# Optimization experiments

Hardware: AMD Instinct MI355X
Metric: run time of the kernel (lower is better)

The kernel has to match this reference:

```python
import jax, jax.numpy as jnp
import numpy as np

CONF = 0.3      # confidence threshold (NMS.conf)
IOU = 0.6       # IoU threshold (NMS.iou)
MAX_WH = 4096.0 # class-offset trick for per-class NMS
K = 2048        # max candidates entering NMS (yolov5-style cap)
MAX_DET = 300   # max detections kept per image (fixed output size)


def setup_inputs() -> dict:
    key = jax.random.key(0)
    kxy, kwh, kobj, kcls = jax.random.split(key, 4)
    B, N, NC = 8, 25200, 80
    # realistic raw predictions: xywh in pixel units for a 640x640 image
    xy = jax.random.uniform(kxy, (B, N, 2), minval=0.0, maxval=640.0)
    wh = jax.random.uniform(kwh, (B, N, 2), minval=2.0, maxval=160.0)
    obj = jax.random.uniform(kobj, (B, N, 1))
    cls = jax.random.uniform(kcls, (B, N, NC))
    x = jnp.concatenate([xy, wh, obj, cls], axis=-1)  # [B, N, 5+NC]
    return {"x": x}


def _xywh2xyxy(b):
    xy, half = b[..., :2], b[..., 2:4] * 0.5
    return jnp.concatenate([xy - half, xy + half], axis=-1)


def _pairwise_iou(boxes):  # boxes: [K, 4] xyxy -> [K, K]
    lt = jnp.maximum(boxes[:, None, :2], boxes[None, :, :2])
    rb = jnp.minimum(boxes[:, None, 2:], boxes[None, :, 2:])
    inter = jnp.clip(rb - lt, 0.0).prod(-1)
    area = (boxes[:, 2] - boxes[:, 0]) * (boxes[:, 3] - boxes[:, 1])
    return inter / (area[:, None] + area[None, :] - inter + 1e-9)


def _nms_single(pred):  # pred: [N, 5+NC]
    obj = pred[:, 4]
    cls_conf = pred[:, 5:] * obj[:, None]          # conf = obj * cls prob
    conf = cls_conf.max(-1)
    cls_id = jnp.argmax(cls_conf, -1)
    valid = (obj > CONF) & (conf > CONF)           # candidate + final threshold
    boxes = _xywh2xyxy(pred[:, :4])
    scores = jnp.where(valid, conf, -1.0)
    top_s, idx = jax.lax.top_k(scores, K)          # cap candidates, sorted desc
    boxes_k = boxes[idx]
    cls_k = cls_id[idx]
    valid_k = top_s > 0.0
    # offset boxes by class so NMS is per-class
    shifted = boxes_k + cls_k[:, None].astype(boxes_k.dtype) * MAX_WH
    iou = _pairwise_iou(shifted)                   # [K, K]
    order = jnp.arange(K)

    def body(keep, i):  # greedy suppression in score order
        active = keep[i] & valid_k[i]
        sup = (iou[i] > IOU) & (order > i)
        keep = jnp.where(active, keep & ~sup, keep)
        return keep, None

    keep, _ = jax.lax.scan(body, jnp.ones((K,), bool), order)
    keep = keep & valid_k
    final_s = jnp.where(keep, top_s, -1.0)
    det_s, det_i = jax.lax.top_k(final_s, MAX_DET)
    dets = jnp.concatenate(
        [boxes_k[det_i], top_s[det_i][:, None],
         cls_k[det_i][:, None].astype(boxes_k.dtype)], axis=-1)  # [MAX_DET, 6]
    return dets, det_s > 0.0


def reference(x):
    # returns (dets [B, MAX_DET, 6] = xyxy,conf,cls ; valid mask [B, MAX_DET])
    return jax.vmap(_nms_single)(x)
```

## Files before the change

### kernel.cpp

```cpp
#include <hip/hip_runtime.h>
#include <hip/hip_bf16.h>

#define B 8
#define N 25200
#define ROW 85
#define NC 80
#define K 2048
#define MAXDET 300
#define NBUCKET 16384
#define CAND_CAP 4096
#define NCHUNK 32
#define STILE 64

__global__ void __launch_bounds__(256)
nms_score_kernel(const float* __restrict__ x,
                 float* __restrict__ scores,
                 int* __restrict__ cls_id) {
    int b = blockIdx.y;
    int i0 = blockIdx.x * STILE;
    int rows = N - i0; if (rows > STILE) rows = STILE;
    __shared__ float lx[STILE * ROW];
    {
        const float4* s4 = (const float4*)(x + ((size_t)b * N + i0) * ROW);
        float4* d4 = (float4*)lx;
        int nv = rows * ROW / 4;
        for (int k = threadIdx.x; k < nv; k += 256) d4[k] = s4[k];
    }
    __syncthreads();
    int g = threadIdx.x >> 2;
    int q = threadIdx.x & 3;
    if (g >= rows) return;
    const float* p = lx + g * ROW;
    float obj = p[4];
    float best = -1e30f;
    int bc = 127;
    if (obj > 0.3f) {
        #pragma unroll
        for (int k = 0; k < 20; ++k) {
            int c = q + 4 * k;
            float v = __fmul_rn(p[5 + c], obj);
            if (v > best) { best = v; bc = c; }
        }
    }
    #pragma unroll
    for (int m = 1; m < 4; m <<= 1) {
        float ov = __shfl_xor(best, m, 64);
        int   oc = __shfl_xor(bc, m, 64);
        if (ov > best || (ov == best && oc < bc)) { best = ov; bc = oc; }
    }
    if (q == 0) {
        int i = i0 + g;
        float score = (obj > 0.3f && best > 0.3f) ? best : -1.0f;
        scores[b * N + i] = score;
        cls_id[b * N + i] = (bc == 127) ? 0 : bc;
    }
}

__global__ void __launch_bounds__(1024, 1)
nms_select_kernel(const float* __restrict__ scores,
                  const float* __restrict__ x,
                  const int* __restrict__ cls_id,
                  float* __restrict__ top_s,
                  float* __restrict__ boxes,
                  int* __restrict__ clsk,
                  float* __restrict__ shifted,
                  float* __restrict__ area,
                  unsigned long long* __restrict__ keepbits) {
    __shared__ unsigned loff[NBUCKET];
    __shared__ unsigned lcnt16[NBUCKET / 2];
    __shared__ unsigned long long lk[CAND_CAP];
    __shared__ unsigned wsum[16];

    int b = blockIdx.x;
    int t = threadIdx.x;
    int ln = t & 63, wv = t >> 6;
    constexpr int NITER = (N + 1023) / 1024;

    if (t < NCHUNK) keepbits[b * NCHUNK + t] = 0ULL;

    {
        uint4 z = {0u, 0u, 0u, 0u};
        uint4* d1 = (uint4*)loff;
        for (int k = t; k < NBUCKET / 4; k += 1024) d1[k] = z;
        uint4* d2 = (uint4*)lcnt16;
        for (int k = t; k < NBUCKET / 8; k += 1024) d2[k] = z;
    }
    for (int k = t; k < CAND_CAP; k += 1024) lk[k] = 0ULL;
    __syncthreads();

    float sreg[NITER];
    #pragma unroll
    for (int r = 0; r < NITER; ++r) {
        int i = t + r * 1024;
        float s = (i < N) ? scores[b * N + i] : -1.0f;
        sreg[r] = s;
        if (s > 0.0f) {
            int q = (int)(__fmul_rn(s, 16384.0f));
            if (q > NBUCKET - 1) q = NBUCKET - 1;
            atomicAdd(&loff[q], 1u);
        }
    }
    __syncthreads();

    unsigned v[16];
    int base_j = t * 16;
    unsigned A4 = (unsigned)(NBUCKET - 16 - base_j) / 4;
    {
        uint4 u0 = ((uint4*)loff)[A4 + 0];
        uint4 u1 = ((uint4*)loff)[A4 + 1];
        uint4 u2 = ((uint4*)loff)[A4 + 2];
        uint4 u3 = ((uint4*)loff)[A4 + 3];
        unsigned u[16] = {u0.x,u0.y,u0.z,u0.w, u1.x,u1.y,u1.z,u1.w,
                          u2.x,u2.y,u2.z,u2.w, u3.x,u3.y,u3.z,u3.w};
        #pragma unroll
        for (int k = 0; k < 16; ++k) v[k] = u[15 - k];
    }
    unsigned S = 0;
    #pragma unroll
    for (int k = 0; k < 16; ++k) S += v[k];
    unsigned pref = S;
    #pragma unroll
    for (int o = 1; o < 64; o <<= 1) { unsigned u = __shfl_up(pref, o, 64); if (ln >= o) pref += u; }
    if (ln == 63) wsum[wv] = pref;
    __syncthreads();
    unsigned wbase = 0;
    for (int w = 0; w < wv; ++w) wbase += wsum[w];
    unsigned running = wbase + pref - S;
    {
        unsigned o[16];
        #pragma unroll
        for (int k = 0; k < 16; ++k) { o[15 - k] = running; running += v[k]; }
        ((uint4*)loff)[A4 + 0] = make_uint4(o[0],  o[1],  o[2],  o[3]);
        ((uint4*)loff)[A4 + 1] = make_uint4(o[4],  o[5],  o[6],  o[7]);
        ((uint4*)loff)[A4 + 2] = make_uint4(o[8],  o[9],  o[10], o[11]);
        ((uint4*)loff)[A4 + 3] = make_uint4(o[12], o[13], o[14], o[15]);
    }
    __syncthreads();

    #pragma unroll
    for (int r = 0; r < NITER; ++r) {
        float s = sreg[r];
        if (s > 0.0f) {
            int i = t + r * 1024;
            int q = (int)(__fmul_rn(s, 16384.0f));
            if (q > NBUCKET - 1) q = NBUCKET - 1;
            unsigned start = loff[q];
            if (start < CAND_CAP) {
                unsigned sh = (q & 1) * 16;
                unsigned old = atomicAdd(&lcnt16[q >> 1], 1u << sh);
                unsigned rank = (old >> sh) & 0xFFFFu;
                unsigned pos = start + rank;
                if (pos < CAND_CAP) {
                    unsigned long long key =
                        ((unsigned long long)__float_as_uint(s) << 32) | (unsigned)(~i);
                    lk[pos] = key;
                }
            }
        }
    }
    __syncthreads();

    for (int q = t; q < NBUCKET; q += 1024) {
        unsigned start = loff[q];
        if (start < CAND_CAP) {
            unsigned c = (lcnt16[q >> 1] >> ((q & 1) * 16)) & 0xFFFFu;
            unsigned m = c;
            if (m > CAND_CAP - start) m = CAND_CAP - start;
            if (m >= 2) {
                for (unsigned a = start + 1; a < start + m; ++a) {
                    unsigned long long kv = lk[a];
                    unsigned p2 = a;
                    while (p2 > start && lk[p2 - 1] < kv) { lk[p2] = lk[p2 - 1]; --p2; }
                    lk[p2] = kv;
                }
            }
        }
    }
    __syncthreads();

    for (int r = t; r < K; r += 1024) {
        unsigned long long key = lk[r];
        float s;
        int idx;
        float x1, y1, x2, y2;
        int c;
        if (key == 0ULL) {
            s = -1.0f; x1 = y1 = x2 = y2 = 0.0f; c = 0;
        } else {
            s = __uint_as_float((unsigned)(key >> 32));
            idx = (int)(~(unsigned)key);
            const float* p = x + ((size_t)b * N + idx) * ROW;
            float cx = p[0], cy = p[1], w = p[2], h = p[3];
            float hx = __fmul_rn(w, 0.5f);
            float hy = __fmul_rn(h, 0.5f);
            x1 = __fsub_rn(cx, hx); y1 = __fsub_rn(cy, hy);
            x2 = __fadd_rn(cx, hx); y2 = __fadd_rn(cy, hy);
            c = cls_id[b * N + idx];
        }
        int o = b * K + r;
        top_s[o] = s;
        boxes[o * 4 + 0] = x1; boxes[o * 4 + 1] = y1;
        boxes[o * 4 + 2] = x2; boxes[o * 4 + 3] = y2;
        clsk[o] = c;
        float sh = __fmul_rn((float)c, 4096.0f);
        float sx1 = __fadd_rn(x1, sh), sy1 = __fadd_rn(y1, sh);
        float sx2 = __fadd_rn(x2, sh), sy2 = __fadd_rn(y2, sh);
        shifted[o * 4 + 0] = sx1; shifted[o * 4 + 1] = sy1;
        shifted[o * 4 + 2] = sx2; shifted[o * 4 + 3] = sy2;
        area[o] = __fmul_rn(__fsub_rn(sx2, sx1), __fsub_rn(sy2, sy1));
    }
}

__global__ void __launch_bounds__(64)
nms_class_kernel(const float* __restrict__ top_s,
                 const int* __restrict__ clsk,
                 const float* __restrict__ shifted,
                 const float* __restrict__ area,
                 unsigned long long* __restrict__ keepbits) {
    int c = blockIdx.x, b = blockIdx.y;
    int t = threadIdx.x;
    unsigned long long below = (t == 0) ? 0ULL : (~0ULL >> (64 - t));

    __shared__ int srank[K];
    __shared__ unsigned long long skeep[NCHUNK];

    int n = 0;
    for (int ch = 0; ch < NCHUNK; ++ch) {
        int r = ch * 64 + t;
        bool sel = (clsk[b * K + r] == c) && (top_s[b * K + r] > 0.0f);
        unsigned long long m = __ballot(sel);
        if (sel) srank[n + __popcll(m & below)] = r;
        n += __popcll(m);
    }
    __syncthreads();
    if (n == 0) return;

    if (n <= 64) {
        float x1 = 0.f, y1 = 0.f, x2 = 0.f, y2 = 0.f, ar = 0.f;
        int r = -1;
        if (t < n) {
            r = srank[t];
            const float* sb = shifted + ((size_t)b * K + r) * 4;
            x1 = sb[0]; y1 = sb[1]; x2 = sb[2]; y2 = sb[3];
            ar = area[b * K + r];
        }
        unsigned long long keepw = (n == 64) ? ~0ULL : ((1ULL << n) - 1ULL);
        for (int i = 0; i < n; ++i) {
            if (!((keepw >> i) & 1ULL)) continue;
            float bx1 = __shfl(x1, i, 64), by1 = __shfl(y1, i, 64);
            float bx2 = __shfl(x2, i, 64), by2 = __shfl(y2, i, 64);
            float ba  = __shfl(ar, i, 64);
            bool cond = false;
            if (t > i && t < n) {
                float lx = fmaxf(bx1, x1), ly = fmaxf(by1, y1);
                float rx = fminf(bx2, x2), ry = fminf(by2, y2);
                float w = fmaxf(__fsub_rn(rx, lx), 0.0f);
                float h = fmaxf(__fsub_rn(ry, ly), 0.0f);
                float inter = __fmul_rn(w, h);
                float denom = __fadd_rn(__fsub_rn(__fadd_rn(ba, ar), inter), 1e-9f);
                cond = __fdiv_rn(inter, denom) > 0.6f;
            }
            keepw &= ~__ballot(cond);
        }
        if (t < n && ((keepw >> t) & 1ULL))
            atomicOr(&keepbits[b * NCHUNK + (r >> 6)], 1ULL << (r & 63));
        return;
    }

    for (int w = t; w < NCHUNK; w += 64) {
        int lo = w * 64;
        unsigned long long vw;
        if (n >= lo + 64)      vw = ~0ULL;
        else if (n <= lo)      vw = 0ULL;
        else                   vw = (1ULL << (n - lo)) - 1ULL;
        skeep[w] = vw;
    }
    __syncthreads();
    for (int i = 0; i < n; ++i) {
        if (!((skeep[i >> 6] >> (i & 63)) & 1ULL)) continue;
        int ri = srank[i];
        const float* sbi = shifted + ((size_t)b * K + ri) * 4;
        float bx1 = sbi[0], by1 = sbi[1], bx2 = sbi[2], by2 = sbi[3];
        float ba = area[b * K + ri];
        int jb_hi = (n - 1) >> 6;
        for (int jb2 = (i + 1) >> 6; jb2 <= jb_hi; ++jb2) {
            int j = jb2 * 64 + t;
            bool cond = false;
            if (j > i && j < n) {
                int rj = srank[j];
                const float* sbj = shifted + ((size_t)b * K + rj) * 4;
                float x1 = sbj[0], y1 = sbj[1], x2 = sbj[2], y2 = sbj[3];
                float arj = area[b * K + rj];
                float lx = fmaxf(bx1, x1), ly = fmaxf(by1, y1);
                float rx = fminf(bx2, x2), ry = fminf(by2, y2);
                float w = fmaxf(__fsub_rn(rx, lx), 0.0f);
                float h = fmaxf(__fsub_rn(ry, ly), 0.0f);
                float inter = __fmul_rn(w, h);
                float denom = __fadd_rn(__fsub_rn(__fadd_rn(ba, arj), inter), 1e-9f);
                cond = __fdiv_rn(inter, denom) > 0.6f;
            }
            unsigned long long sup = __ballot(cond);
            if (t == 0) skeep[jb2] &= ~sup;
        }
        __syncthreads();
    }
    for (int j = t; j < n; j += 64) {
        if ((skeep[j >> 6] >> (j & 63)) & 1ULL) {
            int r = srank[j];
            atomicOr(&keepbits[b * NCHUNK + (r >> 6)], 1ULL << (r & 63));
        }
    }
}

__global__ void __launch_bounds__(64)
nms_out_kernel(const unsigned long long* __restrict__ keepbits,
               const float* __restrict__ top_s,
               const float* __restrict__ boxes,
               const int* __restrict__ clsk,
               float* __restrict__ out) {
    int b = blockIdx.x;
    int lane = threadIdx.x;
    __shared__ unsigned long long kept[NCHUNK];
    if (lane < NCHUNK) kept[lane] = keepbits[b * NCHUNK + lane];
    __syncthreads();

    int total = 0;
    for (int c = 0; c < NCHUNK; ++c) total += __popcll(kept[c]);

    float* dets  = out + (size_t)b * MAXDET * 6;
    float* flags = out + (size_t)B * MAXDET * 6 + (size_t)b * MAXDET;
    unsigned long long below = (lane == 0) ? 0ULL : (~0ULL >> (64 - lane));
    int kc = 0, nc2 = 0;
    for (int c = 0; c < NCHUNK; ++c) {
        int i = c * 64 + lane;
        unsigned long long m = kept[c];
        bool k = ((m >> lane) & 1ULL) != 0ULL;
        int pc = __popcll(m);
        int slot = k ? (kc + __popcll(m & below))
                     : (total + nc2 + __popcll((~m) & below));
        if (slot < MAXDET) {
            int o = b * K + i;
            dets[slot * 6 + 0] = boxes[o * 4 + 0];
            dets[slot * 6 + 1] = boxes[o * 4 + 1];
            dets[slot * 6 + 2] = boxes[o * 4 + 2];
            dets[slot * 6 + 3] = boxes[o * 4 + 3];
            dets[slot * 6 + 4] = top_s[o];
            dets[slot * 6 + 5] = (float)clsk[o];
            flags[slot] = k ? 1.0f : 0.0f;
        }
        kc += pc;
        nc2 += 64 - pc;
    }
}

extern "C" void kernel_launch(void* const* d_in, const int* in_sizes, int n_in,
                              void* d_out, int out_size, void* d_ws, size_t ws_size,
                              hipStream_t stream) {
    const float* x = (const float*)d_in[0];
    float* out = (float*)d_out;

    char* ws = (char*)d_ws;
    size_t off = 0;
    auto alloc = [&](size_t bytes) -> void* {
        void* p = ws + off;
        off += bytes;
        off = (off + 255) & ~(size_t)255;
        return p;
    };

    float*    scores = (float*)    alloc((size_t)B * N * 4);
    int*      cls_id = (int*)      alloc((size_t)B * N * 4);
    float*    top_s  = (float*)    alloc((size_t)B * K * 4);
    float*    boxes  = (float*)    alloc((size_t)B * K * 4 * 4);
    int*      clsk   = (int*)      alloc((size_t)B * K * 4);
    float*    shifted= (float*)    alloc((size_t)B * K * 4 * 4);
    float*    area   = (float*)    alloc((size_t)B * K * 4);
    unsigned long long* keepbits = (unsigned long long*) alloc((size_t)B * NCHUNK * 8);
    (void)ws_size;

    nms_score_kernel<<<dim3((N + STILE - 1) / STILE, B), 256, 0, stream>>>(x, scores, cls_id);
    nms_select_kernel<<<B, 1024, 0, stream>>>(scores, x, cls_id,
                                              top_s, boxes, clsk, shifted, area, keepbits);
    nms_class_kernel<<<dim3(NC, B), 64, 0, stream>>>(top_s, clsk, shifted, area, keepbits);
    nms_out_kernel<<<B, 64, 0, stream>>>(keepbits, top_s, boxes, clsk, out);
}
```

Baseline: 145.4 us.

## Fuse select, per-class NMS and output into one LDS-resident kernel

Merges the candidate selection, per-class greedy NMS and output compaction kernels into a single 1024-thread block per image. Intermediate boxes, scores and keep bits stay in shared memory through unions, removing three launches and their global round trips. Each of the 16 waves now handles five classes instead of one block per class, so per-class parallelism drops from 640 blocks to 8 blocks of 16 waves. Classes with more than 64 candidates scan all K entries serially, which could be slow if such classes occur.

```diff
diff --git a/kernel.cpp b/kernel.cpp
--- a/kernel.cpp
+++ b/kernel.cpp
@@ -57,35 +57,45 @@
 }
 
 __global__ void __launch_bounds__(1024, 1)
-nms_select_kernel(const float* __restrict__ scores,
-                  const float* __restrict__ x,
-                  const int* __restrict__ cls_id,
-                  float* __restrict__ top_s,
-                  float* __restrict__ boxes,
-                  int* __restrict__ clsk,
-                  float* __restrict__ shifted,
-                  float* __restrict__ area,
-                  unsigned long long* __restrict__ keepbits) {
-    __shared__ unsigned loff[NBUCKET];
-    __shared__ unsigned lcnt16[NBUCKET / 2];
-    __shared__ unsigned long long lk[CAND_CAP];
+nms_fused_kernel(const float* __restrict__ scores,
+                 const float* __restrict__ x,
+                 const int* __restrict__ cls_id,
+                 float* __restrict__ out) {
+    __shared__ __align__(16) union {
+        struct { unsigned loff[NBUCKET]; unsigned lcnt16[NBUCKET / 2]; } s1;
+        struct {
+            float sx1[K], sy1[K], sx2[K], sy2[K];
+            float bx1[K], by1[K], bx2[K], by2[K];
+            float sar[K];
+            float ssc[K];
+            int   scl[K];
+        } s2;
+    } U;
+    __shared__ __align__(16) union {
+        unsigned long long lk[CAND_CAP];
+        struct {
+            int tmp64[16][64];
+            unsigned long long wmemb[16][NCHUNK];
+            unsigned long long wkeep[16][NCHUNK];
+            unsigned kept32[2 * NCHUNK];
+        } s3;
+    } V;
     __shared__ unsigned wsum[16];
 
     int b = blockIdx.x;
     int t = threadIdx.x;
     int ln = t & 63, wv = t >> 6;
+    unsigned long long below = (ln == 0) ? 0ULL : (~0ULL >> (64 - ln));
     constexpr int NITER = (N + 1023) / 1024;
-
-    if (t < NCHUNK) keepbits[b * NCHUNK + t] = 0ULL;
 
     {
         uint4 z = {0u, 0u, 0u, 0u};
-        uint4* d1 = (uint4*)loff;
+        uint4* d1 = (uint4*)U.s1.loff;
         for (int k = t; k < NBUCKET / 4; k += 1024) d1[k] = z;
-        uint4* d2 = (uint4*)lcnt16;
+        uint4* d2 = (uint4*)U.s1.lcnt16;
         for (int k = t; k < NBUCKET / 8; k += 1024) d2[k] = z;
     }
-    for (int k = t; k < CAND_CAP; k += 1024) lk[k] = 0ULL;
+    for (int k = t; k < CAND_CAP; k += 1024) V.lk[k] = 0ULL;
     __syncthreads();
 
     float sreg[NITER];
@@ -97,7 +107,7 @@
         if (s > 0.0f) {
             int q = (int)(__fmul_rn(s, 16384.0f));
             if (q > NBUCKET - 1) q = NBUCKET - 1;
-            atomicAdd(&loff[q], 1u);
+            atomicAdd(&U.s1.loff[q], 1u);
         }
     }
     __syncthreads();
@@ -106,10 +116,10 @@
     int base_j = t * 16;
     unsigned A4 = (unsigned)(NBUCKET - 16 - base_j) / 4;
     {
-        uint4 u0 = ((uint4*)loff)[A4 + 0];
-        uint4 u1 = ((uint4*)loff)[A4 + 1];
-        uint4 u2 = ((uint4*)loff)[A4 + 2];
-        uint4 u3 = ((uint4*)loff)[A4 + 3];
+        uint4 u0 = ((uint4*)U.s1.loff)[A4 + 0];
+        uint4 u1 = ((uint4*)U.s1.loff)[A4 + 1];
+        uint4 u2 = ((uint4*)U.s1.loff)[A4 + 2];
+        uint4 u3 = ((uint4*)U.s1.loff)[A4 + 3];
         unsigned u[16] = {u0.x,u0.y,u0.z,u0.w, u1.x,u1.y,u1.z,u1.w,
                           u2.x,u2.y,u2.z,u2.w, u3.x,u3.y,u3.z,u3.w};
         #pragma unroll
@@ -130,10 +140,10 @@
         unsigned o[16];
         #pragma unroll
         for (int k = 0; k < 16; ++k) { o[15 - k] = running; running += v[k]; }
-        ((uint4*)loff)[A4 + 0] = make_uint4(o[0],  o[1],  o[2],  o[3]);
-        ((uint4*)loff)[A4 + 1] = make_uint4(o[4],  o[5],  o[6],  o[7]);
-        ((uint4*)loff)[A4 + 2] = make_uint4(o[8],  o[9],  o[10], o[11]);
-        ((uint4*)loff)[A4 + 3] = make_uint4(o[12], o[13], o[14], o[15]);
+        ((uint4*)U.s1.loff)[A4 + 0] = make_uint4(o[0],  o[1],  o[2],  o[3]);
+        ((uint4*)U.s1.loff)[A4 + 1] = make_uint4(o[4],  o[5],  o[6],  o[7]);
+        ((uint4*)U.s1.loff)[A4 + 2] = make_uint4(o[8],  o[9],  o[10], o[11]);
+        ((uint4*)U.s1.loff)[A4 + 3] = make_uint4(o[12], o[13], o[14], o[15]);
     }
     __syncthreads();
 
@@ -144,16 +154,16 @@
             int i = t + r * 1024;
             int q = (int)(__fmul_rn(s, 16384.0f));
             if (q > NBUCKET - 1) q = NBUCKET - 1;
-            unsigned start = loff[q];
+            unsigned start = U.s1.loff[q];
             if (start < CAND_CAP) {
                 unsigned sh = (q & 1) * 16;
-                unsigned old = atomicAdd(&lcnt16[q >> 1], 1u << sh);
+                unsigned old = atomicAdd(&U.s1.lcnt16[q >> 1], 1u << sh);
                 unsigned rank = (old >> sh) & 0xFFFFu;
                 unsigned pos = start + rank;
                 if (pos < CAND_CAP) {
                     unsigned long long key =
                         ((unsigned long long)__float_as_uint(s) << 32) | (unsigned)(~i);
-                    lk[pos] = key;
+                    V.lk[pos] = key;
                 }
             }
         }
@@ -161,17 +171,17 @@
     __syncthreads();
 
     for (int q = t; q < NBUCKET; q += 1024) {
-        unsigned start = loff[q];
+        unsigned start = U.s1.loff[q];
         if (start < CAND_CAP) {
-            unsigned c = (lcnt16[q >> 1] >> ((q & 1) * 16)) & 0xFFFFu;
+            unsigned c = (U.s1.lcnt16[q >> 1] >> ((q & 1) * 16)) & 0xFFFFu;
             unsigned m = c;
             if (m > CAND_CAP - start) m = CAND_CAP - start;
             if (m >= 2) {
                 for (unsigned a = start + 1; a < start + m; ++a) {
-                    unsigned long long kv = lk[a];
+                    unsigned long long kv = V.lk[a];
                     unsigned p2 = a;
-                    while (p2 > start && lk[p2 - 1] < kv) { lk[p2] = lk[p2 - 1]; --p2; }
-                    lk[p2] = kv;
+                    while (p2 > start && V.lk[p2 - 1] < kv) { V.lk[p2] = V.lk[p2 - 1]; --p2; }
+                    V.lk[p2] = kv;
                 }
             }
         }
@@ -179,7 +189,7 @@
     __syncthreads();
 
     for (int r = t; r < K; r += 1024) {
-        unsigned long long key = lk[r];
+        unsigned long long key = V.lk[r];
         float s;
         int idx;
         float x1, y1, x2, y2;
@@ -197,159 +207,134 @@
             x2 = __fadd_rn(cx, hx); y2 = __fadd_rn(cy, hy);
             c = cls_id[b * N + idx];
         }
-        int o = b * K + r;
-        top_s[o] = s;
-        boxes[o * 4 + 0] = x1; boxes[o * 4 + 1] = y1;
-        boxes[o * 4 + 2] = x2; boxes[o * 4 + 3] = y2;
-        clsk[o] = c;
+        U.s2.ssc[r] = s;
+        U.s2.bx1[r] = x1; U.s2.by1[r] = y1;
+        U.s2.bx2[r] = x2; U.s2.by2[r] = y2;
+        U.s2.scl[r] = c;
         float sh = __fmul_rn((float)c, 4096.0f);
         float sx1 = __fadd_rn(x1, sh), sy1 = __fadd_rn(y1, sh);
         float sx2 = __fadd_rn(x2, sh), sy2 = __fadd_rn(y2, sh);
-        shifted[o * 4 + 0] = sx1; shifted[o * 4 + 1] = sy1;
-        shifted[o * 4 + 2] = sx2; shifted[o * 4 + 3] = sy2;
-        area[o] = __fmul_rn(__fsub_rn(sx2, sx1), __fsub_rn(sy2, sy1));
-    }
-}
-
-__global__ void __launch_bounds__(64)
-nms_class_kernel(const float* __restrict__ top_s,
-                 const int* __restrict__ clsk,
-                 const float* __restrict__ shifted,
-                 const float* __restrict__ area,
-                 unsigned long long* __restrict__ keepbits) {
-    int c = blockIdx.x, b = blockIdx.y;
-    int t = threadIdx.x;
-    unsigned long long below = (t == 0) ? 0ULL : (~0ULL >> (64 - t));
-
-    __shared__ int srank[K];
-    __shared__ unsigned long long skeep[NCHUNK];
-
-    int n = 0;
-    for (int ch = 0; ch < NCHUNK; ++ch) {
-        int r = ch * 64 + t;
-        bool sel = (clsk[b * K + r] == c) && (top_s[b * K + r] > 0.0f);
-        unsigned long long m = __ballot(sel);
-        if (sel) srank[n + __popcll(m & below)] = r;
-        n += __popcll(m);
-    }
-    __syncthreads();
-    if (n == 0) return;
-
-    if (n <= 64) {
-        float x1 = 0.f, y1 = 0.f, x2 = 0.f, y2 = 0.f, ar = 0.f;
-        int r = -1;
-        if (t < n) {
-            r = srank[t];
-            const float* sb = shifted + ((size_t)b * K + r) * 4;
-            x1 = sb[0]; y1 = sb[1]; x2 = sb[2]; y2 = sb[3];
-            ar = area[b * K + r];
-        }
-        unsigned long long keepw = (n == 64) ? ~0ULL : ((1ULL << n) - 1ULL);
-        for (int i = 0; i < n; ++i) {
-            if (!((keepw >> i) & 1ULL)) continue;
-            float bx1 = __shfl(x1, i, 64), by1 = __shfl(y1, i, 64);
-            float bx2 = __shfl(x2, i, 64), by2 = __shfl(y2, i, 64);
-            float ba  = __shfl(ar, i, 64);
-            bool cond = false;
-            if (t > i && t < n) {
-                float lx = fmaxf(bx1, x1), ly = fmaxf(by1, y1);
-                float rx = fminf(bx2, x2), ry = fminf(by2, y2);
-                float w = fmaxf(__fsub_rn(rx, lx), 0.0f);
-                float h = fmaxf(__fsub_rn(ry, ly), 0.0f);
-                float inter = __fmul_rn(w, h);
-                float denom = __fadd_rn(__fsub_rn(__fadd_rn(ba, ar), inter), 1e-9f);
-                cond = __fdiv_rn(inter, denom) > 0.6f;
-            }
-            keepw &= ~__ballot(cond);
-        }
-        if (t < n && ((keepw >> t) & 1ULL))
-            atomicOr(&keepbits[b * NCHUNK + (r >> 6)], 1ULL << (r & 63));
-        return;
-    }
-
-    for (int w = t; w < NCHUNK; w += 64) {
-        int lo = w * 64;
-        unsigned long long vw;
-        if (n >= lo + 64)      vw = ~0ULL;
-        else if (n <= lo)      vw = 0ULL;
-        else                   vw = (1ULL << (n - lo)) - 1ULL;
-        skeep[w] = vw;
-    }
-    __syncthreads();
-    for (int i = 0; i < n; ++i) {
-        if (!((skeep[i >> 6] >> (i & 63)) & 1ULL)) continue;
-        int ri = srank[i];
-        const float* sbi = shifted + ((size_t)b * K + ri) * 4;
-        float bx1 = sbi[0], by1 = sbi[1], bx2 = sbi[2], by2 = sbi[3];
-        float ba = area[b * K + ri];
-        int jb_hi = (n - 1) >> 6;
-        for (int jb2 = (i + 1) >> 6; jb2 <= jb_hi; ++jb2) {
-            int j = jb2 * 64 + t;
-            bool cond = false;
-            if (j > i && j < n) {
-                int rj = srank[j];
-                const float* sbj = shifted + ((size_t)b * K + rj) * 4;
-                float x1 = sbj[0], y1 = sbj[1], x2 = sbj[2], y2 = sbj[3];
-                float arj = area[b * K + rj];
-                float lx = fmaxf(bx1, x1), ly = fmaxf(by1, y1);
-                float rx = fminf(bx2, x2), ry = fminf(by2, y2);
-                float w = fmaxf(__fsub_rn(rx, lx), 0.0f);
-                float h = fmaxf(__fsub_rn(ry, ly), 0.0f);
-                float inter = __fmul_rn(w, h);
-                float denom = __fadd_rn(__fsub_rn(__fadd_rn(ba, arj), inter), 1e-9f);
-                cond = __fdiv_rn(inter, denom) > 0.6f;
-            }
-            unsigned long long sup = __ballot(cond);
-            if (t == 0) skeep[jb2] &= ~sup;
-        }
-        __syncthreads();
-    }
-    for (int j = t; j < n; j += 64) {
-        if ((skeep[j >> 6] >> (j & 63)) & 1ULL) {
-            int r = srank[j];
-            atomicOr(&keepbits[b * NCHUNK + (r >> 6)], 1ULL << (r & 63));
-        }
-    }
-}
-
-__global__ void __launch_bounds__(64)
-nms_out_kernel(const unsigned long long* __restrict__ keepbits,
-               const float* __restrict__ top_s,
-               const float* __restrict__ boxes,
-               const int* __restrict__ clsk,
-               float* __restrict__ out) {
-    int b = blockIdx.x;
-    int lane = threadIdx.x;
-    __shared__ unsigned long long kept[NCHUNK];
-    if (lane < NCHUNK) kept[lane] = keepbits[b * NCHUNK + lane];
-    __syncthreads();
-
-    int total = 0;
-    for (int c = 0; c < NCHUNK; ++c) total += __popcll(kept[c]);
-
-    float* dets  = out + (size_t)b * MAXDET * 6;
-    float* flags = out + (size_t)B * MAXDET * 6 + (size_t)b * MAXDET;
-    unsigned long long below = (lane == 0) ? 0ULL : (~0ULL >> (64 - lane));
-    int kc = 0, nc2 = 0;
-    for (int c = 0; c < NCHUNK; ++c) {
-        int i = c * 64 + lane;
-        unsigned long long m = kept[c];
-        bool k = ((m >> lane) & 1ULL) != 0ULL;
-        int pc = __popcll(m);
-        int slot = k ? (kc + __popcll(m & below))
-                     : (total + nc2 + __popcll((~m) & below));
-        if (slot < MAXDET) {
-            int o = b * K + i;
-            dets[slot * 6 + 0] = boxes[o * 4 + 0];
-            dets[slot * 6 + 1] = boxes[o * 4 + 1];
-            dets[slot * 6 + 2] = boxes[o * 4 + 2];
-            dets[slot * 6 + 3] = boxes[o * 4 + 3];
-            dets[slot * 6 + 4] = top_s[o];
-            dets[slot * 6 + 5] = (float)clsk[o];
-            flags[slot] = k ? 1.0f : 0.0f;
-        }
-        kc += pc;
-        nc2 += 64 - pc;
+        U.s2.sx1[r] = sx1; U.s2.sy1[r] = sy1;
+        U.s2.sx2[r] = sx2; U.s2.sy2[r] = sy2;
+        U.s2.sar[r] = __fmul_rn(__fsub_rn(sx2, sx1), __fsub_rn(sy2, sy1));
+    }
+    __syncthreads();
+    if (t < 2 * NCHUNK) V.s3.kept32[t] = 0u;
+    __syncthreads();
+
+    for (int c = wv; c < NC; c += 16) {
+        int n = 0;
+        for (int ch = 0; ch < NCHUNK; ++ch) {
+            int r = ch * 64 + ln;
+            bool sel = (U.s2.scl[r] == c) && (U.s2.ssc[r] > 0.0f);
+            unsigned long long m = __ballot(sel);
+            int pos = n + __popcll(m & below);
+            if (sel && pos < 64) V.s3.tmp64[wv][pos] = r;
+            n += __popcll(m);
+        }
+        if (n == 0) continue;
+
+        if (n <= 64) {
+            int r = -1;
+            float x1 = 0.f, y1 = 0.f, x2 = 0.f, y2 = 0.f, ar = 0.f;
+            if (ln < n) {
+                r = V.s3.tmp64[wv][ln];
+                x1 = U.s2.sx1[r]; y1 = U.s2.sy1[r];
+                x2 = U.s2.sx2[r]; y2 = U.s2.sy2[r];
+                ar = U.s2.sar[r];
+            }
+            unsigned long long keepw = (n == 64) ? ~0ULL : ((1ULL << n) - 1ULL);
+            for (int i = 0; i < n; ++i) {
+                if (!((keepw >> i) & 1ULL)) continue;
+                float bx1 = __shfl(x1, i, 64), by1 = __shfl(y1, i, 64);
+                float bx2 = __shfl(x2, i, 64), by2 = __shfl(y2, i, 64);
+                float ba  = __shfl(ar, i, 64);
+                bool cond = false;
+                if (ln > i && ln < n) {
+                    float lx = fmaxf(bx1, x1), ly = fmaxf(by1, y1);
+                    float rx = fminf(bx2, x2), ry = fminf(by2, y2);
+                    float w = fmaxf(__fsub_rn(rx, lx), 0.0f);
+                    float h = fmaxf(__fsub_rn(ry, ly), 0.0f);
+                    float inter = __fmul_rn(w, h);
+                    float denom = __fadd_rn(__fsub_rn(__fadd_rn(ba, ar), inter), 1e-9f);
+                    cond = __fdiv_rn(inter, denom) > 0.6f;
+                }
+                keepw &= ~__ballot(cond);
+            }
+            if (ln < n && ((keepw >> ln) & 1ULL))
+                atomicOr(&V.s3.kept32[r >> 5], 1u << (r & 31));
+        } else {
+            unsigned long long* memb = V.s3.wmemb[wv];
+            unsigned long long* keep = V.s3.wkeep[wv];
+            for (int ch = 0; ch < NCHUNK; ++ch) {
+                int r = ch * 64 + ln;
+                bool sel = (U.s2.scl[r] == c) && (U.s2.ssc[r] > 0.0f);
+                unsigned long long m = __ballot(sel);
+                if (ln == 0) { memb[ch] = m; keep[ch] = m; }
+            }
+            for (int i = 0; i < K; ++i) {
+                unsigned long long bi = 1ULL << (i & 63);
+                if (!(memb[i >> 6] & keep[i >> 6] & bi)) continue;
+                float bx1 = U.s2.sx1[i], by1 = U.s2.sy1[i];
+                float bx2 = U.s2.sx2[i], by2 = U.s2.sy2[i];
+                float ba  = U.s2.sar[i];
+                for (int ch = i >> 6; ch < NCHUNK; ++ch) {
+                    int r = ch * 64 + ln;
+                    bool cond = false;
+                    if (r > i && ((memb[ch] >> ln) & 1ULL)) {
+                        float lx = fmaxf(bx1, U.s2.sx1[r]);
+                        float ly = fmaxf(by1, U.s2.sy1[r]);
+                        float rx = fminf(bx2, U.s2.sx2[r]);
+                        float ry = fminf(by2, U.s2.sy2[r]);
+                        float w = fmaxf(__fsub_rn(rx, lx), 0.0f);
+                        float h = fmaxf(__fsub_rn(ry, ly), 0.0f);
+                        float inter = __fmul_rn(w, h);
+                        float denom = __fadd_rn(__fsub_rn(__fadd_rn(ba, U.s2.sar[r]), inter), 1e-9f);
+                        cond = __fdiv_rn(inter, denom) > 0.6f;
+                    }
+                    unsigned long long sup = __ballot(cond);
+                    if (ln == 0) keep[ch] &= ~sup;
+                }
+            }
+            for (int ch = 0; ch < NCHUNK; ++ch) {
+                int r = ch * 64 + ln;
+                if ((keep[ch] >> ln) & 1ULL)
+                    atomicOr(&V.s3.kept32[r >> 5], 1u << (r & 31));
+            }
+        }
+    }
+    __syncthreads();
+
+    if (wv == 0) {
+        int total = 0;
+        for (int c = 0; c < NCHUNK; ++c) {
+            unsigned long long m = (unsigned long long)V.s3.kept32[2 * c]
+                                 | ((unsigned long long)V.s3.kept32[2 * c + 1] << 32);
+            total += __popcll(m);
+        }
+        float* dets  = out + (size_t)b * MAXDET * 6;
+        float* flags = out + (size_t)B * MAXDET * 6 + (size_t)b * MAXDET;
+        int kc = 0, nc2 = 0;
+        for (int c = 0; c < NCHUNK; ++c) {
+            int i = c * 64 + ln;
+            unsigned long long m = (unsigned long long)V.s3.kept32[2 * c]
+                                 | ((unsigned long long)V.s3.kept32[2 * c + 1] << 32);
+            bool k = ((m >> ln) & 1ULL) != 0ULL;
+            int pc = __popcll(m);
+            int slot = k ? (kc + __popcll(m & below))
+                         : (total + nc2 + __popcll((~m) & below));
+            if (slot < MAXDET) {
+                dets[slot * 6 + 0] = U.s2.bx1[i];
+                dets[slot * 6 + 1] = U.s2.by1[i];
+                dets[slot * 6 + 2] = U.s2.bx2[i];
+                dets[slot * 6 + 3] = U.s2.by2[i];
+                dets[slot * 6 + 4] = U.s2.ssc[i];
+                dets[slot * 6 + 5] = (float)U.s2.scl[i];
+                flags[slot] = k ? 1.0f : 0.0f;
+            }
+            kc += pc;
+            nc2 += 64 - pc;
+        }
     }
 }
 
@@ -368,19 +353,10 @@
         return p;
     };
 
-    float*    scores = (float*)    alloc((size_t)B * N * 4);
-    int*      cls_id = (int*)      alloc((size_t)B * N * 4);
-    float*    top_s  = (float*)    alloc((size_t)B * K * 4);
-    float*    boxes  = (float*)    alloc((size_t)B * K * 4 * 4);
-    int*      clsk   = (int*)      alloc((size_t)B * K * 4);
-    float*    shifted= (float*)    alloc((size_t)B * K * 4 * 4);
-    float*    area   = (float*)    alloc((size_t)B * K * 4);
-    unsigned long long* keepbits = (unsigned long long*) alloc((size_t)B * NCHUNK * 8);
+    float* scores = (float*) alloc((size_t)B * N * 4);
+    int*   cls_id = (int*)   alloc((size_t)B * N * 4);
     (void)ws_size;
 
     nms_score_kernel<<<dim3((N + STILE - 1) / STILE, B), 256, 0, stream>>>(x, scores, cls_id);
-    nms_select_kernel<<<B, 1024, 0, stream>>>(scores, x, cls_id,
-                                              top_s, boxes, clsk, shifted, area, keepbits);
-    nms_class_kernel<<<dim3(NC, B), 64, 0, stream>>>(top_s, clsk, shifted, area, keepbits);
-    nms_out_kernel<<<B, 64, 0, stream>>>(keepbits, top_s, boxes, clsk, out);
+    nms_fused_kernel<<<B, 1024, 0, stream>>>(scores, x, cls_id, out);
 }
```

Result: slower. 184.2 us (+26.7%).

## Build score histogram in score kernel with global atomics instead of select kernel

Applied to the files above, without the earlier changes.

Moves the per-image score bucket histogram out of the single-block-per-image select kernel and into the highly parallel score kernel, using global atomics into a per-image histogram buffer. The select kernel then reads the histogram straight from global memory for its prefix scan, skipping its serial pass over all scores and the LDS histogram clear. It adds a memset of the histogram buffer before each launch, and global atomic contention on popular buckets.

```diff
diff --git a/kernel.cpp b/kernel.cpp
--- a/kernel.cpp
+++ b/kernel.cpp
@@ -15,7 +15,8 @@
 __global__ void __launch_bounds__(256)
 nms_score_kernel(const float* __restrict__ x,
                  float* __restrict__ scores,
-                 int* __restrict__ cls_id) {
+                 int* __restrict__ cls_id,
+                 unsigned* __restrict__ hist) {
     int b = blockIdx.y;
     int i0 = blockIdx.x * STILE;
     int rows = N - i0; if (rows > STILE) rows = STILE;
@@ -53,6 +54,11 @@
         float score = (obj > 0.3f && best > 0.3f) ? best : -1.0f;
         scores[b * N + i] = score;
         cls_id[b * N + i] = (bc == 127) ? 0 : bc;
+        if (score > 0.0f) {
+            int qb = (int)(__fmul_rn(score, 16384.0f));
+            if (qb > NBUCKET - 1) qb = NBUCKET - 1;
+            atomicAdd(&hist[b * NBUCKET + qb], 1u);
+        }
     }
 }
 
@@ -60,6 +66,7 @@
 nms_select_kernel(const float* __restrict__ scores,
                   const float* __restrict__ x,
                   const int* __restrict__ cls_id,
+                  const unsigned* __restrict__ hist,
                   float* __restrict__ top_s,
                   float* __restrict__ boxes,
                   int* __restrict__ clsk,
@@ -80,36 +87,20 @@
 
     {
         uint4 z = {0u, 0u, 0u, 0u};
-        uint4* d1 = (uint4*)loff;
-        for (int k = t; k < NBUCKET / 4; k += 1024) d1[k] = z;
         uint4* d2 = (uint4*)lcnt16;
         for (int k = t; k < NBUCKET / 8; k += 1024) d2[k] = z;
     }
     for (int k = t; k < CAND_CAP; k += 1024) lk[k] = 0ULL;
-    __syncthreads();
-
-    float sreg[NITER];
-    #pragma unroll
-    for (int r = 0; r < NITER; ++r) {
-        int i = t + r * 1024;
-        float s = (i < N) ? scores[b * N + i] : -1.0f;
-        sreg[r] = s;
-        if (s > 0.0f) {
-            int q = (int)(__fmul_rn(s, 16384.0f));
-            if (q > NBUCKET - 1) q = NBUCKET - 1;
-            atomicAdd(&loff[q], 1u);
-        }
-    }
-    __syncthreads();
 
     unsigned v[16];
     int base_j = t * 16;
     unsigned A4 = (unsigned)(NBUCKET - 16 - base_j) / 4;
     {
-        uint4 u0 = ((uint4*)loff)[A4 + 0];
-        uint4 u1 = ((uint4*)loff)[A4 + 1];
-        uint4 u2 = ((uint4*)loff)[A4 + 2];
-        uint4 u3 = ((uint4*)loff)[A4 + 3];
+        const uint4* gh = (const uint4*)(hist + (size_t)b * NBUCKET);
+        uint4 u0 = gh[A4 + 0];
+        uint4 u1 = gh[A4 + 1];
+        uint4 u2 = gh[A4 + 2];
+        uint4 u3 = gh[A4 + 3];
         unsigned u[16] = {u0.x,u0.y,u0.z,u0.w, u1.x,u1.y,u1.z,u1.w,
                           u2.x,u2.y,u2.z,u2.w, u3.x,u3.y,u3.z,u3.w};
         #pragma unroll
@@ -137,6 +128,12 @@
     }
     __syncthreads();
 
+    float sreg[NITER];
+    #pragma unroll
+    for (int r = 0; r < NITER; ++r) {
+        int i = t + r * 1024;
+        sreg[r] = (i < N) ? scores[b * N + i] : -1.0f;
+    }
     #pragma unroll
     for (int r = 0; r < NITER; ++r) {
         float s = sreg[r];
@@ -376,10 +373,12 @@
     float*    shifted= (float*)    alloc((size_t)B * K * 4 * 4);
     float*    area   = (float*)    alloc((size_t)B * K * 4);
     unsigned long long* keepbits = (unsigned long long*) alloc((size_t)B * NCHUNK * 8);
+    unsigned* hist   = (unsigned*) alloc((size_t)B * NBUCKET * 4);
     (void)ws_size;
 
-    nms_score_kernel<<<dim3((N + STILE - 1) / STILE, B), 256, 0, stream>>>(x, scores, cls_id);
-    nms_select_kernel<<<B, 1024, 0, stream>>>(scores, x, cls_id,
+    hipMemsetAsync(hist, 0, (size_t)B * NBUCKET * 4, stream);
+    nms_score_kernel<<<dim3((N + STILE - 1) / STILE, B), 256, 0, stream>>>(x, scores, cls_id, hist);
+    nms_select_kernel<<<B, 1024, 0, stream>>>(scores, x, cls_id, hist,
                                               top_s, boxes, clsk, shifted, area, keepbits);
     nms_class_kernel<<<dim3(NC, B), 64, 0, stream>>>(top_s, clsk, shifted, area, keepbits);
     nms_out_kernel<<<B, 64, 0, stream>>>(keepbits, top_s, boxes, clsk, out);
```

Result: no change. 144.5 us (-0.6%).
